# Kernel optimization log

Measured on AMD Instinct MI355X. Metric: run time of the kernel, lower is better.

The kernel has to match this reference:

```python
import jax, jax.numpy as jnp
import numpy as np

N_NODES = 100000
N_EDGES = 1600000
N_GRAPHS = 64
D_IN = 3
HIDDEN = 256
N_CLASSES = 10
NEG_SLOPE = 0.01  # torch F.leaky_relu default


def gcn_conv(x, W, b, src, dst, n_nodes):
    """GCNConv: D^{-1/2}(A+I)D^{-1/2} X W + b with self-loops."""
    h = x @ W  # [N, H]
    ones = jnp.ones(src.shape[0], h.dtype)
    deg = jax.ops.segment_sum(ones, dst, num_segments=n_nodes) + 1.0  # +1 self-loop
    dinv = jax.lax.rsqrt(deg)
    coef = dinv[src] * dinv[dst]  # [E]
    agg = jax.ops.segment_sum(h[src] * coef[:, None], dst, num_segments=n_nodes)
    agg = agg + h * (1.0 / deg)[:, None]  # self-loop contribution (norm = 1/deg)
    return agg + b


def leaky_relu(v):
    return jnp.where(v >= 0, v, NEG_SLOPE * v)


def setup_inputs() -> dict:
    key = jax.random.key(0)
    ks = jax.random.split(key, 12)
    x = jax.random.normal(ks[0], (N_NODES, D_IN), dtype=jnp.float32)
    edge_index = jax.random.randint(ks[1], (2, N_EDGES), 0, N_NODES, dtype=jnp.int32)
    batch = jnp.sort(jax.random.randint(ks[2], (N_NODES,), 0, N_GRAPHS, dtype=jnp.int32))
    s1 = 1.0 / np.sqrt(D_IN)
    s2 = 1.0 / np.sqrt(HIDDEN)
    W1 = jax.random.uniform(ks[3], (D_IN, HIDDEN), jnp.float32, -s1, s1)
    b1 = jnp.zeros((HIDDEN,), jnp.float32)
    W2 = jax.random.uniform(ks[4], (HIDDEN, HIDDEN), jnp.float32, -s2, s2)
    b2 = jnp.zeros((HIDDEN,), jnp.float32)
    W3 = jax.random.uniform(ks[5], (HIDDEN, HIDDEN), jnp.float32, -s2, s2)
    b3 = jnp.zeros((HIDDEN,), jnp.float32)
    Wc = jax.random.uniform(ks[6], (HIDDEN, N_CLASSES), jnp.float32, -s2, s2)
    bc = jax.random.uniform(ks[7], (N_CLASSES,), jnp.float32, -s2, s2)
    return {"x": x, "edge_index": edge_index, "batch": batch,
            "W1": W1, "b1": b1, "W2": W2, "b2": b2, "W3": W3, "b3": b3,
            "Wc": Wc, "bc": bc}


def reference(x, edge_index, batch, W1, b1, W2, b2, W3, b3, Wc, bc):
    src, dst = edge_index[0], edge_index[1]
    h = leaky_relu(gcn_conv(x, W1, b1, src, dst, N_NODES))
    h = leaky_relu(gcn_conv(h, W2, b2, src, dst, N_NODES))
    h = leaky_relu(gcn_conv(h, W3, b3, src, dst, N_NODES))
    # global mean pool over graphs
    sums = jax.ops.segment_sum(h, batch, num_segments=N_GRAPHS)
    cnt = jax.ops.segment_sum(jnp.ones((N_NODES,), h.dtype), batch, num_segments=N_GRAPHS)
    pooled = sums / jnp.maximum(cnt, 1.0)[:, None]  # [G, H]
    logits = pooled @ Wc + bc
    return jax.nn.softmax(logits, axis=1)
```

## Files before the change

kernel.cpp:

```cpp
#include <hip/hip_runtime.h>
#include <hip/hip_bf16.h>
#include <hip/hip_fp16.h>
#include <cstdint>
#include <cstddef>

#define N_NODES   100000
#define N_EDGES   1600000
#define N_GRAPHS  64
#define HIDDEN    256
#define N_CLASSES 10
#define NEG_SLOPE 0.01f

#define E_PAD    (N_EDGES + 8 * N_NODES)
#define N_RANGES 8
#define R_SIZE   ((N_NODES + N_RANGES - 1) / N_RANGES)
#define CHUNK    2048
#define GEMM_BLOCKS 391

typedef __attribute__((ext_vector_type(4))) float f32x4;
typedef __attribute__((ext_vector_type(2))) float f32x2;

__device__ __forceinline__ float bf2f(unsigned short u) {
    return __uint_as_float(((unsigned int)u) << 16);
}

__device__ __forceinline__ unsigned char f2fp8(float v) {
    return (unsigned char)(__builtin_amdgcn_cvt_pk_fp8_f32(v, v, 0, false) & 0xff);
}

__device__ __forceinline__ unsigned int rec_pack(int s, float c) {
    __half h = __float2half(c);
    unsigned short hb = reinterpret_cast<const __half_raw*>(&h)->x;
    return ((unsigned int)hb << 17) | (unsigned int)s;
}
__device__ __forceinline__ float rec_coef(unsigned int u) {
    __half_raw hr; hr.x = (unsigned short)(u >> 17);
    return __half2float(*reinterpret_cast<const __half*>(&hr));
}

__global__ __launch_bounds__(256) void k_deg_hist(const int* __restrict__ dst, int* __restrict__ cnt) {
    int b = blockIdx.x;
    int r = b & (N_RANGES - 1);
    int lo = r * R_SIZE, hi = lo + R_SIZE;
    int e0 = (b >> 3) * CHUNK + threadIdx.x * 8;
    if (e0 >= N_EDGES) return;
    int4 da = *(const int4*)(dst + e0);
    int4 db = *(const int4*)(dst + e0 + 4);
    int d[8] = {da.x, da.y, da.z, da.w, db.x, db.y, db.z, db.w};
#pragma unroll
    for (int j = 0; j < 8; ++j) {
        if (d[j] >= lo && d[j] < hi) atomicAdd(&cnt[d[j]], 1);
    }
}

__global__ void k_graph_bounds(const int* __restrict__ batch,
                               int* __restrict__ gstart, int* __restrict__ gcnt) {
    int g = threadIdx.x;
    int lo = 0, hi = N_NODES;
    while (lo < hi) { int mid = (lo + hi) >> 1; if (batch[mid] < g) lo = mid + 1; else hi = mid; }
    __shared__ int sh[N_GRAPHS + 1];
    sh[g] = lo;
    if (g == 0) sh[N_GRAPHS] = N_NODES;
    __syncthreads();
    gstart[g] = sh[g];
    gcnt[g]   = sh[g + 1] - sh[g];
}

__global__ void k_dinv_xpad(const int* __restrict__ cnt, const float* __restrict__ x,
                            float* __restrict__ dinv, float4* __restrict__ xp) {
    int i = blockIdx.x * 256 + threadIdx.x;
    if (i < N_NODES) {
        dinv[i] = rsqrtf((float)cnt[i] + 1.0f);
        xp[i] = make_float4(x[i * 3 + 0], x[i * 3 + 1], x[i * 3 + 2], 0.f);
    }
}

__global__ void k_scanA(const int* __restrict__ cnt, int* __restrict__ out, int* __restrict__ bsum) {
    __shared__ int sh[256];
    int tid = threadIdx.x;
    int base = blockIdx.x * 1024 + tid * 4;
    int v[4]; int s = 0;
#pragma unroll
    for (int i = 0; i < 4; i++) {
        int idx = base + i;
        v[i] = (idx < N_NODES) ? ((cnt[idx] + 7) & ~7) : 0;
        s += v[i];
    }
    sh[tid] = s; __syncthreads();
    for (int off = 1; off < 256; off <<= 1) {
        int t = (tid >= off) ? sh[tid - off] : 0;
        __syncthreads();
        sh[tid] += t;
        __syncthreads();
    }
    int excl = sh[tid] - s;
    if (tid == 255) bsum[blockIdx.x] = sh[255];
#pragma unroll
    for (int i = 0; i < 4; i++) { int idx = base + i; if (idx < N_NODES) out[idx] = excl; excl += v[i]; }
}

__global__ void k_scanB(int* __restrict__ bsum, int nb) {
    __shared__ int sh[128];
    int tid = threadIdx.x;
    int v = (tid < nb) ? bsum[tid] : 0;
    sh[tid] = v; __syncthreads();
    for (int off = 1; off < 128; off <<= 1) {
        int t = (tid >= off) ? sh[tid - off] : 0;
        __syncthreads();
        sh[tid] += t;
        __syncthreads();
    }
    if (tid < nb) bsum[tid] = sh[tid] - v;
}

__global__ void k_scanC(int* __restrict__ off_arr, const int* __restrict__ bsum,
                        int* __restrict__ cursor, const int* __restrict__ cnt,
                        unsigned int* __restrict__ rec) {
    int i = blockIdx.x * 256 + threadIdx.x;
    if (i < N_NODES) {
        int v = off_arr[i] + bsum[i >> 10];
        off_arr[i] = v;
        cursor[i]  = v;
        int c  = cnt[i];
        int cp = (c + 7) & ~7;
        for (int p = v + c; p < v + cp; ++p) rec[p] = 0u;
        if (i == N_NODES - 1) off_arr[N_NODES] = v + cp;
    }
}

__global__ __launch_bounds__(256) void k_fill(const int* __restrict__ src, const int* __restrict__ dst,
                                              const float* __restrict__ dinv,
                                              int* __restrict__ cursor, unsigned int* __restrict__ rec) {
    int b = blockIdx.x;
    int r = b & (N_RANGES - 1);
    int lo = r * R_SIZE, hi = lo + R_SIZE;
    int e0 = (b >> 3) * CHUNK + threadIdx.x * 8;
    if (e0 >= N_EDGES) return;
    int4 da = *(const int4*)(dst + e0);
    int4 db = *(const int4*)(dst + e0 + 4);
    int d[8] = {da.x, da.y, da.z, da.w, db.x, db.y, db.z, db.w};
#pragma unroll
    for (int j = 0; j < 8; ++j) {
        if (d[j] >= lo && d[j] < hi) {
            int s = src[e0 + j];
            float c = dinv[s] * dinv[d[j]];
            int p = atomicAdd(&cursor[d[j]], 1);
            rec[p] = rec_pack(s, c);
        }
    }
}

__global__ void k_wprep(const float* __restrict__ W, unsigned char* __restrict__ Wswz) {
    int n = blockIdx.x; int k = threadIdx.x;
    unsigned char v = f2fp8(W[k * HIDDEN + n]);
    int k0 = k >> 5, nt = n >> 4;
    int lane = (((k >> 3) & 3) << 4) | (n & 15);
    int j = k & 7;
    Wswz[(size_t)(((k0 * 16) + nt) * 64 + lane) * 8 + j] = v;
}

__global__ void k_agg3(const float4* __restrict__ xp, const int* __restrict__ off,
                       const unsigned int* __restrict__ rec, const float* __restrict__ dinv,
                       float4* __restrict__ ax) {
    int i = blockIdx.x * 256 + threadIdx.x;
    if (i >= N_NODES) return;
    float di = dinv[i];
    float selfc = di * di;
    float4 xi = xp[i];
    float a0 = xi.x * selfc, a1 = xi.y * selfc, a2 = xi.z * selfc;
    int e = off[i], e1 = off[i + 1];
    for (; e < e1; e += 4) {
        uint4 rr = *(const uint4*)(rec + e);
        int s0 = rr.x & 0x1ffff, s1 = rr.y & 0x1ffff, s2 = rr.z & 0x1ffff, s3 = rr.w & 0x1ffff;
        float c0 = rec_coef(rr.x), c1 = rec_coef(rr.y), c2 = rec_coef(rr.z), c3 = rec_coef(rr.w);
        float4 x0 = xp[s0], x1 = xp[s1], x2 = xp[s2], x3 = xp[s3];
        a0 += c0 * x0.x + c1 * x1.x + c2 * x2.x + c3 * x3.x;
        a1 += c0 * x0.y + c1 * x1.y + c2 * x2.y + c3 * x3.y;
        a2 += c0 * x0.z + c1 * x1.z + c2 * x2.z + c3 * x3.z;
    }
    ax[i] = make_float4(a0, a1, a2, 0.f);
}

__global__ void k_l1(const float4* __restrict__ ax, const float* __restrict__ W1,
                     const float* __restrict__ b1, unsigned char* __restrict__ out) {
    int node = blockIdx.x; int c = threadIdx.x;
    float4 a = ax[node];
    float v = a.x * W1[c] + a.y * W1[HIDDEN + c] + a.z * W1[2 * HIDDEN + c] + b1[c];
    v = v >= 0.f ? v : NEG_SLOPE * v;
    out[(size_t)node * HIDDEN + c] = f2fp8(v);
}

__global__ __launch_bounds__(512, 2) void k_gemm_mfma(const unsigned char* __restrict__ A,
                                                      const unsigned char* __restrict__ Wswz,
                                                      unsigned char* __restrict__ C, int M) {
    __shared__ long Bs[8192];
    int tid = threadIdx.x;
    {
        const float4* gsrc = (const float4*)Wswz;
        float4* ldst = (float4*)Bs;
#pragma unroll
        for (int i = 0; i < 8; ++i) ldst[tid + 512 * i] = gsrc[tid + 512 * i];
    }
    __syncthreads();
    int lane = tid & 63, wv = tid >> 6;
    int quad = lane >> 4, r = lane & 15;
    int nstrips = M >> 4;
    for (int s = blockIdx.x * 8 + wv; s < nstrips; s += gridDim.x * 8) {
        int m0 = s * 16;
        const long* Ab = (const long*)(A + (size_t)(m0 + r) * HIDDEN) + quad;
        long af[8];
#pragma unroll
        for (int k0 = 0; k0 < 8; ++k0) af[k0] = Ab[k0 * 4];
#pragma unroll
        for (int half = 0; half < 2; ++half) {
            f32x4 acc[8];
#pragma unroll
            for (int i = 0; i < 8; i++) acc[i] = (f32x4){0.f, 0.f, 0.f, 0.f};
#pragma unroll
            for (int k0 = 0; k0 < 8; ++k0) {
#pragma unroll
                for (int nt = 0; nt < 8; ++nt) {
                    long b = Bs[(k0 * 16 + half * 8 + nt) * 64 + lane];
                    acc[nt] = __builtin_amdgcn_mfma_f32_16x16x32_fp8_fp8(af[k0], b, acc[nt], 0, 0, 0);
                }
            }
#pragma unroll
            for (int nt = 0; nt < 8; ++nt) {
#pragma unroll
                for (int i = 0; i < 4; ++i) {
                    int row = m0 + quad * 4 + i;
                    C[(size_t)row * HIDDEN + (half * 8 + nt) * 16 + r] = f2fp8(acc[nt][i]);
                }
            }
        }
    }
}

__global__ __launch_bounds__(256) void k_agg(const unsigned char* __restrict__ h,
                                             const float* __restrict__ bias,
                                             const int* __restrict__ off, const unsigned int* __restrict__ rec,
                                             const float* __restrict__ dinv,
                                             unsigned char* __restrict__ out) {
    int node = (blockIdx.x * 256 + threadIdx.x) >> 6;
    int lane = threadIdx.x & 63;
    if (node >= N_NODES) return;
    float di = dinv[node];
    float selfc = di * di;
    unsigned int hv = *(const unsigned int*)(h + (size_t)node * HIDDEN + lane * 4);
    f32x2 hlo = __builtin_amdgcn_cvt_pk_f32_fp8(hv, false);
    f32x2 hhi = __builtin_amdgcn_cvt_pk_f32_fp8(hv, true);
    float4 bv = ((const float4*)bias)[lane];
    float4 acc = make_float4(bv.x + hlo.x * selfc, bv.y + hlo.y * selfc,
                             bv.z + hhi.x * selfc, bv.w + hhi.y * selfc);
    int e = off[node], e1 = off[node + 1];
    for (; e < e1; e += 8) {
        uint4 ra = *(const uint4*)(rec + e);
        uint4 rb = *(const uint4*)(rec + e + 4);
        unsigned int w0 = *(const unsigned int*)(h + (size_t)(ra.x & 0x1ffff) * HIDDEN + lane * 4);
        unsigned int w1 = *(const unsigned int*)(h + (size_t)(ra.y & 0x1ffff) * HIDDEN + lane * 4);
        unsigned int w2 = *(const unsigned int*)(h + (size_t)(ra.z & 0x1ffff) * HIDDEN + lane * 4);
        unsigned int w3 = *(const unsigned int*)(h + (size_t)(ra.w & 0x1ffff) * HIDDEN + lane * 4);
        unsigned int w4 = *(const unsigned int*)(h + (size_t)(rb.x & 0x1ffff) * HIDDEN + lane * 4);
        unsigned int w5 = *(const unsigned int*)(h + (size_t)(rb.y & 0x1ffff) * HIDDEN + lane * 4);
        unsigned int w6 = *(const unsigned int*)(h + (size_t)(rb.z & 0x1ffff) * HIDDEN + lane * 4);
        unsigned int w7 = *(const unsigned int*)(h + (size_t)(rb.w & 0x1ffff) * HIDDEN + lane * 4);
        float c0 = rec_coef(ra.x), c1 = rec_coef(ra.y), c2 = rec_coef(ra.z), c3 = rec_coef(ra.w);
        float c4 = rec_coef(rb.x), c5 = rec_coef(rb.y), c6 = rec_coef(rb.z), c7 = rec_coef(rb.w);
        f32x2 l0 = __builtin_amdgcn_cvt_pk_f32_fp8(w0, false), g0 = __builtin_amdgcn_cvt_pk_f32_fp8(w0, true);
        f32x2 l1 = __builtin_amdgcn_cvt_pk_f32_fp8(w1, false), g1 = __builtin_amdgcn_cvt_pk_f32_fp8(w1, true);
        f32x2 l2 = __builtin_amdgcn_cvt_pk_f32_fp8(w2, false), g2 = __builtin_amdgcn_cvt_pk_f32_fp8(w2, true);
        f32x2 l3 = __builtin_amdgcn_cvt_pk_f32_fp8(w3, false), g3 = __builtin_amdgcn_cvt_pk_f32_fp8(w3, true);
        f32x2 l4 = __builtin_amdgcn_cvt_pk_f32_fp8(w4, false), g4 = __builtin_amdgcn_cvt_pk_f32_fp8(w4, true);
        f32x2 l5 = __builtin_amdgcn_cvt_pk_f32_fp8(w5, false), g5 = __builtin_amdgcn_cvt_pk_f32_fp8(w5, true);
        f32x2 l6 = __builtin_amdgcn_cvt_pk_f32_fp8(w6, false), g6 = __builtin_amdgcn_cvt_pk_f32_fp8(w6, true);
        f32x2 l7 = __builtin_amdgcn_cvt_pk_f32_fp8(w7, false), g7 = __builtin_amdgcn_cvt_pk_f32_fp8(w7, true);
        acc.x += c0 * l0.x + c1 * l1.x + c2 * l2.x + c3 * l3.x
               + c4 * l4.x + c5 * l5.x + c6 * l6.x + c7 * l7.x;
        acc.y += c0 * l0.y + c1 * l1.y + c2 * l2.y + c3 * l3.y
               + c4 * l4.y + c5 * l5.y + c6 * l6.y + c7 * l7.y;
        acc.z += c0 * g0.x + c1 * g1.x + c2 * g2.x + c3 * g3.x
               + c4 * g4.x + c5 * g5.x + c6 * g6.x + c7 * g7.x;
        acc.w += c0 * g0.y + c1 * g1.y + c2 * g2.y + c3 * g3.y
               + c4 * g4.y + c5 * g5.y + c6 * g6.y + c7 * g7.y;
    }
    acc.x = acc.x >= 0.f ? acc.x : NEG_SLOPE * acc.x;
    acc.y = acc.y >= 0.f ? acc.y : NEG_SLOPE * acc.y;
    acc.z = acc.z >= 0.f ? acc.z : NEG_SLOPE * acc.z;
    acc.w = acc.w >= 0.f ? acc.w : NEG_SLOPE * acc.w;
    unsigned int pk = __builtin_amdgcn_cvt_pk_fp8_f32(acc.x, acc.y, 0, false);
    pk = __builtin_amdgcn_cvt_pk_fp8_f32(acc.z, acc.w, pk, true);
    *(unsigned int*)(out + (size_t)node * HIDDEN + lane * 4) = pk;
}

__global__ void k_pool(const unsigned char* __restrict__ h, const int* __restrict__ gstart,
                       const int* __restrict__ gcnt, float* __restrict__ pooled) {
    int g = blockIdx.x, chunk = blockIdx.y, t = threadIdx.x;
    int s = gstart[g], c = gcnt[g];
    int i0 = s + (int)(((long long)c * chunk) / 16);
    int i1 = s + (int)(((long long)c * (chunk + 1)) / 16);
    float acc = 0.f;
    for (int i = i0; i < i1; ++i) {
        f32x2 v = __builtin_amdgcn_cvt_pk_f32_fp8((unsigned int)h[(size_t)i * HIDDEN + t], false);
        acc += v.x;
    }
    atomicAdd(&pooled[g * HIDDEN + t], acc);
}

__global__ void k_head(const float* __restrict__ pooled, const int* __restrict__ gcnt,
                       const float* __restrict__ Wc, const float* __restrict__ bc,
                       float* __restrict__ out) {
    int g = blockIdx.x; int l = threadIdx.x;
    float inv = 1.0f / fmaxf((float)gcnt[g], 1.0f);
    float p[4];
#pragma unroll
    for (int i = 0; i < 4; i++) p[i] = pooled[g * HIDDEN + l + i * 64] * inv;
    __shared__ float logits[N_CLASSES];
#pragma unroll
    for (int j = 0; j < N_CLASSES; j++) {
        float s = 0.f;
#pragma unroll
        for (int i = 0; i < 4; i++) s += p[i] * Wc[(l + i * 64) * N_CLASSES + j];
        for (int o = 32; o > 0; o >>= 1) s += __shfl_down(s, o, 64);
        if (l == 0) logits[j] = s + bc[j];
    }
    __syncthreads();
    if (l == 0) {
        float m = logits[0];
        for (int j = 1; j < N_CLASSES; j++) m = fmaxf(m, logits[j]);
        float e[N_CLASSES]; float sum = 0.f;
        for (int j = 0; j < N_CLASSES; j++) { e[j] = expf(logits[j] - m); sum += e[j]; }
        for (int j = 0; j < N_CLASSES; j++) out[g * N_CLASSES + j] = e[j] / sum;
    }
}

extern "C" void kernel_launch(void* const* d_in, const int* in_sizes, int n_in,
                              void* d_out, int out_size, void* d_ws, size_t ws_size,
                              hipStream_t stream) {
    const float* x     = (const float*)d_in[0];
    const int*   edge  = (const int*)d_in[1];
    const int*   batch = (const int*)d_in[2];
    const float* W1 = (const float*)d_in[3];
    const float* b1 = (const float*)d_in[4];
    const float* W2 = (const float*)d_in[5];
    const float* b2 = (const float*)d_in[6];
    const float* W3 = (const float*)d_in[7];
    const float* b3 = (const float*)d_in[8];
    const float* Wc = (const float*)d_in[9];
    const float* bc = (const float*)d_in[10];
    float* out = (float*)d_out;
    const int* srcp = edge;
    const int* dstp = edge + N_EDGES;

    char* ws = (char*)d_ws;
    size_t off = 0;
    auto alloc = [&](size_t bytes) -> char* {
        char* p = ws + off;
        off += (bytes + 255) & ~(size_t)255;
        return p;
    };
    unsigned char* hA   = (unsigned char*)alloc((size_t)N_NODES * HIDDEN);
    unsigned char* hB   = (unsigned char*)alloc((size_t)N_NODES * HIDDEN);
    unsigned char* Wz2  = (unsigned char*)alloc((size_t)HIDDEN * HIDDEN);
    unsigned char* Wz3  = (unsigned char*)alloc((size_t)HIDDEN * HIDDEN);
    int*   deg_cnt  = (int*)alloc((size_t)N_NODES * 4);
    float* dinv     = (float*)alloc((size_t)N_NODES * 4);
    int*   csr_off  = (int*)alloc((size_t)(N_NODES + 1) * 4);
    int*   cursor   = (int*)alloc((size_t)N_NODES * 4);
    unsigned int* csr_rec = (unsigned int*)alloc((size_t)E_PAD * 4);
    float4* ax      = (float4*)alloc((size_t)N_NODES * 16);
    float4* xp      = (float4*)alloc((size_t)N_NODES * 16);
    int*   gcnt     = (int*)alloc((size_t)N_GRAPHS * 4);
    int*   gstart   = (int*)alloc((size_t)N_GRAPHS * 4);
    float* pooled   = (float*)alloc((size_t)N_GRAPHS * HIDDEN * 4);
    int*   bsum     = (int*)alloc(128 * 4);

    hipMemsetAsync(deg_cnt, 0, (size_t)N_NODES * 4, stream);
    hipMemsetAsync(pooled, 0, (size_t)N_GRAPHS * HIDDEN * 4, stream);

    int nb  = (N_NODES + 255) / 256;
    int sblocks = (N_NODES + 1023) / 1024;
    int fillb = N_RANGES * ((N_EDGES + CHUNK - 1) / CHUNK);

    k_deg_hist<<<fillb, 256, 0, stream>>>(dstp, deg_cnt);
    k_graph_bounds<<<1, 64, 0, stream>>>(batch, gstart, gcnt);
    k_dinv_xpad<<<nb, 256, 0, stream>>>(deg_cnt, x, dinv, xp);
    k_scanA<<<sblocks, 256, 0, stream>>>(deg_cnt, csr_off, bsum);
    k_scanB<<<1, 128, 0, stream>>>(bsum, sblocks);
    k_scanC<<<nb, 256, 0, stream>>>(csr_off, bsum, cursor, deg_cnt, csr_rec);
    k_fill<<<fillb, 256, 0, stream>>>(srcp, dstp, dinv, cursor, csr_rec);
    k_wprep<<<HIDDEN, HIDDEN, 0, stream>>>(W2, Wz2);
    k_wprep<<<HIDDEN, HIDDEN, 0, stream>>>(W3, Wz3);

    k_agg3<<<nb, 256, 0, stream>>>(xp, csr_off, csr_rec, dinv, ax);
    k_l1<<<N_NODES, 256, 0, stream>>>(ax, W1, b1, hA);

    int aggb = (N_NODES + 3) / 4;
    k_gemm_mfma<<<GEMM_BLOCKS, 512, 0, stream>>>(hA, Wz2, hB, N_NODES);
    k_agg<<<aggb, 256, 0, stream>>>(hB, b2, csr_off, csr_rec, dinv, hA);
    k_gemm_mfma<<<GEMM_BLOCKS, 512, 0, stream>>>(hA, Wz3, hB, N_NODES);
    k_agg<<<aggb, 256, 0, stream>>>(hB, b3, csr_off, csr_rec, dinv, hA);
    dim3 pg(N_GRAPHS, 16);
    k_pool<<<pg, 256, 0, stream>>>(hA, gstart, gcnt, pooled);
    k_head<<<N_GRAPHS, 64, 0, stream>>>(pooled, gcnt, Wc, bc, out);
}
```

Before: 539.0 us.

## Partition edges by destination range before histogram and CSR fill

Replaces the 8x-redundant scan of the full edge list in the degree histogram and fill kernels with a single partitioning pass. That pass bins edges into 8 destination-range buckets through shared-memory staging. The histogram kernel then records each edge's rank within its destination, so the fill kernel writes records with no cursor atomics. The buckets and rank bytes reuse the hB buffer as scratch. Ranks are stored in 8 bits, so this assumes in-degree stays below 256, and bucket capacity is fixed per range.

```diff
diff --git a/kernel.cpp b/kernel.cpp
--- a/kernel.cpp
+++ b/kernel.cpp
@@ -14,8 +14,12 @@
 #define E_PAD    (N_EDGES + 8 * N_NODES)
 #define N_RANGES 8
 #define R_SIZE   ((N_NODES + N_RANGES - 1) / N_RANGES)
-#define CHUNK    2048
 #define GEMM_BLOCKS 391
+
+#define PART_EDGES  8192
+#define PART_BLOCKS ((N_EDGES + PART_EDGES - 1) / PART_EDGES)
+#define RB_CHUNKS   108
+#define CAP_R       (RB_CHUNKS * 2048)
 
 typedef __attribute__((ext_vector_type(4))) float f32x4;
 typedef __attribute__((ext_vector_type(2))) float f32x2;
@@ -38,18 +42,115 @@
     return __half2float(*reinterpret_cast<const __half*>(&hr));
 }
 
-__global__ __launch_bounds__(256) void k_deg_hist(const int* __restrict__ dst, int* __restrict__ cnt) {
+__global__ __launch_bounds__(256) void k_partition(const int* __restrict__ src, const int* __restrict__ dst,
+                                                   int* __restrict__ gcur, unsigned int* __restrict__ bucket) {
+    __shared__ int lcnt[8];
+    __shared__ int lbase[8];
+    __shared__ int gbase[8];
+    __shared__ unsigned int stage[PART_EDGES];
+    int tid = threadIdx.x;
+    if (tid < 8) lcnt[tid] = 0;
+    __syncthreads();
+    int e0 = blockIdx.x * PART_EDGES + tid * 8;
+    for (int g = 0; g < 4; ++g) {
+        int e = e0 + g * 2048;
+        if (e < N_EDGES) {
+            int4 da = *(const int4*)(dst + e);
+            int4 db = *(const int4*)(dst + e + 4);
+            int d[8] = {da.x, da.y, da.z, da.w, db.x, db.y, db.z, db.w};
+#pragma unroll
+            for (int j = 0; j < 8; ++j) atomicAdd(&lcnt[d[j] / R_SIZE], 1);
+        }
+    }
+    __syncthreads();
+    if (tid == 0) {
+        int s = 0;
+        for (int r = 0; r < 8; ++r) { lbase[r] = s; s += lcnt[r]; }
+    }
+    __syncthreads();
+    if (tid < 8) {
+        gbase[tid] = atomicAdd(&gcur[tid * 16], lcnt[tid]);
+        lcnt[tid] = lbase[tid];
+    }
+    __syncthreads();
+    for (int g = 0; g < 4; ++g) {
+        int e = e0 + g * 2048;
+        if (e < N_EDGES) {
+            int4 da = *(const int4*)(dst + e);
+            int4 db = *(const int4*)(dst + e + 4);
+            int4 sa = *(const int4*)(src + e);
+            int4 sb = *(const int4*)(src + e + 4);
+            int d[8] = {da.x, da.y, da.z, da.w, db.x, db.y, db.z, db.w};
+            int s[8] = {sa.x, sa.y, sa.z, sa.w, sb.x, sb.y, sb.z, sb.w};
+#pragma unroll
+            for (int j = 0; j < 8; ++j) {
+                int r = d[j] / R_SIZE;
+                int p = atomicAdd(&lcnt[r], 1);
+                stage[p] = ((unsigned int)(d[j] - r * R_SIZE) << 17) | (unsigned int)s[j];
+            }
+        }
+    }
+    __syncthreads();
+    for (int r = 0; r < 8; ++r) {
+        int base = lbase[r], n = lcnt[r] - base, gb = gbase[r];
+        unsigned int* dp = bucket + (size_t)r * CAP_R + gb;
+        for (int k = tid; k < n; k += 256) dp[k] = stage[base + k];
+    }
+}
+
+__global__ __launch_bounds__(256) void k_hist2(const unsigned int* __restrict__ bucket,
+                                               const int* __restrict__ gcur,
+                                               int* __restrict__ cnt, unsigned char* __restrict__ rankb) {
     int b = blockIdx.x;
-    int r = b & (N_RANGES - 1);
-    int lo = r * R_SIZE, hi = lo + R_SIZE;
-    int e0 = (b >> 3) * CHUNK + threadIdx.x * 8;
-    if (e0 >= N_EDGES) return;
-    int4 da = *(const int4*)(dst + e0);
-    int4 db = *(const int4*)(dst + e0 + 4);
-    int d[8] = {da.x, da.y, da.z, da.w, db.x, db.y, db.z, db.w};
+    int r = b & 7, chunk = b >> 3;
+    int n = gcur[r * 16];
+    int i0 = chunk * 2048 + threadIdx.x * 8;
+    if (i0 >= n) return;
+    const unsigned int* bp = bucket + (size_t)r * CAP_R;
+    uint4 ua = *(const uint4*)(bp + i0);
+    uint4 ub = *(const uint4*)(bp + i0 + 4);
+    unsigned int u[8] = {ua.x, ua.y, ua.z, ua.w, ub.x, ub.y, ub.z, ub.w};
+    int lo = r * R_SIZE;
+    int m = n - i0; if (m > 8) m = 8;
+    unsigned long long pk = 0;
 #pragma unroll
     for (int j = 0; j < 8; ++j) {
-        if (d[j] >= lo && d[j] < hi) atomicAdd(&cnt[d[j]], 1);
+        if (j < m) {
+            int d = lo + (int)(u[j] >> 17);
+            unsigned int rk = (unsigned int)atomicAdd(&cnt[d], 1);
+            pk |= (unsigned long long)(rk & 0xff) << (8 * j);
+        }
+    }
+    *(unsigned long long*)(rankb + (size_t)r * CAP_R + i0) = pk;
+}
+
+__global__ __launch_bounds__(256) void k_fill2(const unsigned int* __restrict__ bucket,
+                                               const unsigned char* __restrict__ rankb,
+                                               const int* __restrict__ gcur,
+                                               const float* __restrict__ dinv,
+                                               const int* __restrict__ off,
+                                               unsigned int* __restrict__ rec) {
+    int b = blockIdx.x;
+    int r = b & 7, chunk = b >> 3;
+    int n = gcur[r * 16];
+    int i0 = chunk * 2048 + threadIdx.x * 8;
+    if (i0 >= n) return;
+    const unsigned int* bp = bucket + (size_t)r * CAP_R;
+    uint4 ua = *(const uint4*)(bp + i0);
+    uint4 ub = *(const uint4*)(bp + i0 + 4);
+    unsigned long long rk8 = *(const unsigned long long*)(rankb + (size_t)r * CAP_R + i0);
+    unsigned int u[8] = {ua.x, ua.y, ua.z, ua.w, ub.x, ub.y, ub.z, ub.w};
+    int lo = r * R_SIZE;
+    int m = n - i0; if (m > 8) m = 8;
+#pragma unroll
+    for (int j = 0; j < 8; ++j) {
+        if (j < m) {
+            int s = (int)(u[j] & 0x1ffff);
+            int d = lo + (int)(u[j] >> 17);
+            float c = dinv[s] * dinv[d];
+            int p = off[d] + (int)((rk8 >> (8 * j)) & 0xff);
+            rec[p] = rec_pack(s, c);
+        }
     }
 }
 
@@ -114,39 +215,15 @@
 }
 
 __global__ void k_scanC(int* __restrict__ off_arr, const int* __restrict__ bsum,
-                        int* __restrict__ cursor, const int* __restrict__ cnt,
-                        unsigned int* __restrict__ rec) {
+                        const int* __restrict__ cnt, unsigned int* __restrict__ rec) {
     int i = blockIdx.x * 256 + threadIdx.x;
     if (i < N_NODES) {
         int v = off_arr[i] + bsum[i >> 10];
         off_arr[i] = v;
-        cursor[i]  = v;
         int c  = cnt[i];
         int cp = (c + 7) & ~7;
         for (int p = v + c; p < v + cp; ++p) rec[p] = 0u;
         if (i == N_NODES - 1) off_arr[N_NODES] = v + cp;
-    }
-}
-
-__global__ __launch_bounds__(256) void k_fill(const int* __restrict__ src, const int* __restrict__ dst,
-                                              const float* __restrict__ dinv,
-                                              int* __restrict__ cursor, unsigned int* __restrict__ rec) {
-    int b = blockIdx.x;
-    int r = b & (N_RANGES - 1);
-    int lo = r * R_SIZE, hi = lo + R_SIZE;
-    int e0 = (b >> 3) * CHUNK + threadIdx.x * 8;
-    if (e0 >= N_EDGES) return;
-    int4 da = *(const int4*)(dst + e0);
-    int4 db = *(const int4*)(dst + e0 + 4);
-    int d[8] = {da.x, da.y, da.z, da.w, db.x, db.y, db.z, db.w};
-#pragma unroll
-    for (int j = 0; j < 8; ++j) {
-        if (d[j] >= lo && d[j] < hi) {
-            int s = src[e0 + j];
-            float c = dinv[s] * dinv[d[j]];
-            int p = atomicAdd(&cursor[d[j]], 1);
-            rec[p] = rec_pack(s, c);
-        }
     }
 }
 
@@ -365,7 +442,6 @@
     int*   deg_cnt  = (int*)alloc((size_t)N_NODES * 4);
     float* dinv     = (float*)alloc((size_t)N_NODES * 4);
     int*   csr_off  = (int*)alloc((size_t)(N_NODES + 1) * 4);
-    int*   cursor   = (int*)alloc((size_t)N_NODES * 4);
     unsigned int* csr_rec = (unsigned int*)alloc((size_t)E_PAD * 4);
     float4* ax      = (float4*)alloc((size_t)N_NODES * 16);
     float4* xp      = (float4*)alloc((size_t)N_NODES * 16);
@@ -373,21 +449,27 @@
     int*   gstart   = (int*)alloc((size_t)N_GRAPHS * 4);
     float* pooled   = (float*)alloc((size_t)N_GRAPHS * HIDDEN * 4);
     int*   bsum     = (int*)alloc(128 * 4);
+    int*   gcur     = (int*)alloc(128 * 4);
+
+    unsigned int*  bucket = (unsigned int*)hB;
+    unsigned char* rankb  = (unsigned char*)(hB + (size_t)8 * CAP_R * 4);
 
     hipMemsetAsync(deg_cnt, 0, (size_t)N_NODES * 4, stream);
+    hipMemsetAsync(gcur, 0, 128 * 4, stream);
     hipMemsetAsync(pooled, 0, (size_t)N_GRAPHS * HIDDEN * 4, stream);
 
     int nb  = (N_NODES + 255) / 256;
     int sblocks = (N_NODES + 1023) / 1024;
-    int fillb = N_RANGES * ((N_EDGES + CHUNK - 1) / CHUNK);
-
-    k_deg_hist<<<fillb, 256, 0, stream>>>(dstp, deg_cnt);
+    int rbgrid = RB_CHUNKS * N_RANGES;
+
+    k_partition<<<PART_BLOCKS, 256, 0, stream>>>(srcp, dstp, gcur, bucket);
     k_graph_bounds<<<1, 64, 0, stream>>>(batch, gstart, gcnt);
+    k_hist2<<<rbgrid, 256, 0, stream>>>(bucket, gcur, deg_cnt, rankb);
     k_dinv_xpad<<<nb, 256, 0, stream>>>(deg_cnt, x, dinv, xp);
     k_scanA<<<sblocks, 256, 0, stream>>>(deg_cnt, csr_off, bsum);
     k_scanB<<<1, 128, 0, stream>>>(bsum, sblocks);
-    k_scanC<<<nb, 256, 0, stream>>>(csr_off, bsum, cursor, deg_cnt, csr_rec);
-    k_fill<<<fillb, 256, 0, stream>>>(srcp, dstp, dinv, cursor, csr_rec);
+    k_scanC<<<nb, 256, 0, stream>>>(csr_off, bsum, deg_cnt, csr_rec);
+    k_fill2<<<rbgrid, 256, 0, stream>>>(bucket, rankb, gcur, dinv, csr_off, csr_rec);
     k_wprep<<<HIDDEN, HIDDEN, 0, stream>>>(W2, Wz2);
     k_wprep<<<HIDDEN, HIDDEN, 0, stream>>>(W3, Wz3);
 
```

Measured after the change: 509.3 us. -5.5%, faster.
